# Kernel tuning notes

Measured on AMD Instinct MI355X. Metric: run time of the kernel, lower is better.

The kernel has to match this reference:

```python
import jax, jax.numpy as jnp
import numpy as np

BATCH, LENGTH, IN, STATE, OUT = 8, 4096, 512, 256, 512


def setup_inputs() -> dict:
    key = jax.random.key(0)
    k1, k2, k3, k4, k5 = jax.random.split(key, 5)
    u = jax.random.normal(k1, (BATCH, LENGTH, IN), dtype=jnp.float32)
    x0 = jax.random.normal(k2, (BATCH, STATE), dtype=jnp.float32)
    A = 0.9999 * (2.0 * jax.random.uniform(k3, (STATE,), dtype=jnp.float32) - 1.0)
    B = jax.random.normal(k4, (IN, STATE), dtype=jnp.float32) / (STATE + IN) ** 0.5
    C = jax.random.normal(k5, (STATE, OUT), dtype=jnp.float32) / STATE ** 0.5
    return {"u": u, "x0": x0, "A": A, "B": B, "C": C}


def reference(u, x0, A, B, C):
    L = u.shape[1]
    # A_powers[t, n] = A[n] ** t, shape [L, state]
    A_powers = jnp.power(A[None, :], jnp.arange(L, dtype=u.dtype)[:, None])
    uB = u @ B  # [batch, L, state]
    # FFT convolution; inputs are real so rfft/irfft gives same result as
    # real(ifft(fft*fft)) in the original.
    T = 2 ** int(np.ceil(np.log2(2 * L - 1)))
    Af = jnp.fft.rfft(A_powers, n=T, axis=0)  # [T/2+1, state]
    Uf = jnp.fft.rfft(uB, n=T, axis=1)        # [batch, T/2+1, state]
    x = jnp.fft.irfft(Af[None, :, :] * Uf, n=T, axis=1)[:, :L]  # [batch, L, state]
    # initial-state contribution: A * A_powers * x0
    x = x + A[None, None, :] * A_powers[None, :, :] * x0[:, None, :]
    y = x @ C  # [batch, L, out]
    return (y, x[:, -1])
```

## Files before the change

kernel.cpp:

```cpp
#include <hip/hip_runtime.h>

#define BATCH   8
#define LENGTH  4096
#define IN_DIM  512
#define STATE   256
#define OUT_DIM 512
#define NC      64
#define LC      64

typedef __attribute__((ext_vector_type(8))) short bf16x8;
typedef __attribute__((ext_vector_type(4))) float f32x4;

union FragU { bf16x8 v; unsigned u[4]; };

__device__ __forceinline__ unsigned short bf16_rne(float v) {
    unsigned u = __builtin_bit_cast(unsigned, v);
    unsigned r = (u + 0x7FFFu + ((u >> 16) & 1u)) >> 16;
    return (unsigned short)r;
}
__device__ __forceinline__ float bf16_f(unsigned short h) {
    unsigned u = ((unsigned)h) << 16;
    return __builtin_bit_cast(float, u);
}

__global__ __launch_bounds__(256) void split_T_kernel(
    const float* __restrict__ in, unsigned short* __restrict__ hi,
    unsigned short* __restrict__ lo, int kbits, int Nsrc)
{
    int id = blockIdx.x * 256 + threadIdx.x;
    int k = id & ((1 << kbits) - 1);
    int n = id >> kbits;
    float v = in[(size_t)k * Nsrc + n];
    unsigned short h = bf16_rne(v);
    hi[id] = h;
    lo[id] = bf16_rne(v - bf16_f(h));
}

__global__ __launch_bounds__(512, 4) void gemm_dbuf(
    const float* __restrict__ Af, const unsigned short* __restrict__ Bthi,
    const unsigned short* __restrict__ Btlo, float* __restrict__ Cc,
    int N_, int K)
{
    __shared__ unsigned short lds[2 * 16384];

    const int tid  = threadIdx.x;
    const int wave = tid >> 6;
    const int lane = tid & 63;
    const int n0 = blockIdx.x * 128;
    const int m0 = blockIdx.y * 128;

    const char* gp[4];
    int ldsoff[4], gstep[4];
    #pragma unroll
    for (int t = 0; t < 4; ++t) {
        int gi = wave * 4 + t;
        if (gi < 16) {
            int p = gi * 64 + lane;
            int row = p >> 3, s = p & 7;
            int l = s ^ (row & 7);
            gp[t] = (const char*)(Af + (size_t)(m0 + row) * K + l * 4);
            gstep[t] = 32 * 4;
            ldsoff[t] = gi * 512;
        } else {
            int q2 = (gi - 16) >> 3;
            int pi = gi & 7;
            int p = pi * 64 + lane;
            int row = p >> 2, s = p & 3;
            int l = s ^ ((row >> 1) & 3);
            const unsigned short* base = q2 ? Btlo : Bthi;
            gp[t] = (const char*)(base + (size_t)(n0 + row) * K + l * 8);
            gstep[t] = 32 * 2;
            ldsoff[t] = 8192 + q2 * 4096 + pi * 512;
        }
    }

    const int r = lane & 15, q = lane >> 4;
    const int wm = (wave >> 2) * 64, wn = (wave & 3) * 32;

    int aoff[4][2], boff[2];
    #pragma unroll
    for (int i = 0; i < 4; ++i) {
        int row = wm + i * 16 + r;
        #pragma unroll
        for (int h = 0; h < 2; ++h)
            aoff[i][h] = row * 64 + ((2 * q + h) ^ (row & 7)) * 8;
    }
    #pragma unroll
    for (int j = 0; j < 2; ++j) {
        int row = wn + j * 16 + r;
        boff[j] = row * 32 + (q ^ ((row >> 1) & 3)) * 8;
    }

    f32x4 acc[4][2];
    #pragma unroll
    for (int i = 0; i < 4; ++i)
        #pragma unroll
        for (int j = 0; j < 2; ++j)
            acc[i][j] = (f32x4){0.f, 0.f, 0.f, 0.f};

    #pragma unroll
    for (int t = 0; t < 4; ++t) {
        __builtin_amdgcn_global_load_lds(
            (const __attribute__((address_space(1))) unsigned*)(gp[t]),
            (__attribute__((address_space(3))) unsigned*)(&lds[ldsoff[t]]),
            16, 0, 0);
        gp[t] += gstep[t];
    }

    const int nit = K >> 5;
    for (int it = 0; it < nit; ++it) {
        asm volatile("" ::: "memory");
        __builtin_amdgcn_s_barrier();
        asm volatile("" ::: "memory");
        if (it + 1 < nit) {
            const int bb = ((it + 1) & 1) * 16384;
            #pragma unroll
            for (int t = 0; t < 4; ++t) {
                __builtin_amdgcn_global_load_lds(
                    (const __attribute__((address_space(1))) unsigned*)(gp[t]),
                    (__attribute__((address_space(3))) unsigned*)(&lds[bb + ldsoff[t]]),
                    16, 0, 0);
                gp[t] += gstep[t];
            }
            __builtin_amdgcn_s_waitcnt(0x0F74);
        } else {
            __builtin_amdgcn_s_waitcnt(0x0F70);
        }
        asm volatile("" ::: "memory");
        __builtin_amdgcn_s_barrier();
        asm volatile("" ::: "memory");

        const unsigned short* buf = &lds[(it & 1) * 16384];

        FragU ahi[4], alo[4];
        #pragma unroll
        for (int i = 0; i < 4; ++i) {
            #pragma unroll
            for (int h = 0; h < 2; ++h) {
                float4 f = *(const float4*)(buf + aoff[i][h]);
                unsigned bx = __builtin_bit_cast(unsigned, f.x);
                unsigned by = __builtin_bit_cast(unsigned, f.y);
                unsigned bz = __builtin_bit_cast(unsigned, f.z);
                unsigned bw = __builtin_bit_cast(unsigned, f.w);
                ahi[i].u[h * 2]     = __builtin_amdgcn_perm(by, bx, 0x07060302);
                ahi[i].u[h * 2 + 1] = __builtin_amdgcn_perm(bw, bz, 0x07060302);
                float lx = f.x - __builtin_bit_cast(float, bx & 0xFFFF0000u);
                float ly = f.y - __builtin_bit_cast(float, by & 0xFFFF0000u);
                float lz = f.z - __builtin_bit_cast(float, bz & 0xFFFF0000u);
                float lw = f.w - __builtin_bit_cast(float, bw & 0xFFFF0000u);
                alo[i].u[h * 2]     = __builtin_amdgcn_perm(
                    __builtin_bit_cast(unsigned, ly), __builtin_bit_cast(unsigned, lx), 0x07060302);
                alo[i].u[h * 2 + 1] = __builtin_amdgcn_perm(
                    __builtin_bit_cast(unsigned, lw), __builtin_bit_cast(unsigned, lz), 0x07060302);
            }
        }
        FragU bhi[2], blo[2];
        #pragma unroll
        for (int j = 0; j < 2; ++j) {
            bhi[j].v = *(const bf16x8*)(buf +  8192 + boff[j]);
            blo[j].v = *(const bf16x8*)(buf + 12288 + boff[j]);
        }
        #pragma unroll
        for (int i = 0; i < 4; ++i)
            #pragma unroll
            for (int j = 0; j < 2; ++j) {
                acc[i][j] = __builtin_amdgcn_mfma_f32_16x16x32_bf16(ahi[i].v, bhi[j].v, acc[i][j], 0, 0, 0);
                acc[i][j] = __builtin_amdgcn_mfma_f32_16x16x32_bf16(alo[i].v, bhi[j].v, acc[i][j], 0, 0, 0);
                acc[i][j] = __builtin_amdgcn_mfma_f32_16x16x32_bf16(ahi[i].v, blo[j].v, acc[i][j], 0, 0, 0);
            }
    }

    #pragma unroll
    for (int i = 0; i < 4; ++i) {
        #pragma unroll
        for (int reg = 0; reg < 4; ++reg) {
            int mg = m0 + wm + i * 16 + q * 4 + reg;
            float* dst = Cc + (size_t)mg * N_ + n0 + wn + r;
            dst[0]  = acc[i][0][reg];
            dst[16] = acc[i][1][reg];
        }
    }
}

__global__ __launch_bounds__(256) void scan_carry(
    const float* __restrict__ uB, const float* __restrict__ A,
    float* __restrict__ carry)
{
    const int b = blockIdx.x;
    const int c = blockIdx.y;
    const int n = threadIdx.x;
    const float a = A[n];
    const float* p = uB + ((size_t)b * LENGTH + (size_t)c * LC) * STATE + n;
    float s = 0.f;
    #pragma unroll 8
    for (int j = 0; j < LC; ++j) s = a * s + p[(size_t)j * STATE];
    carry[((size_t)b * NC + c) * STATE + n] = s;
}

__global__ __launch_bounds__(256) void scan_apply(
    const float* __restrict__ uB, const float* __restrict__ A,
    const float* __restrict__ carry, const float* __restrict__ x0,
    float* __restrict__ x, float* __restrict__ x_last)
{
    const int b = blockIdx.x;
    const int c = blockIdx.y;
    const int n = threadIdx.x;
    const float a = A[n];
    float a2 = a * a, a4 = a2 * a2, a8 = a4 * a4, a16 = a8 * a8, a32 = a16 * a16;
    const float aLC = a32 * a32;

    float s = x0[(size_t)b * STATE + n];
    for (int d = 0; d < c; ++d)
        s = aLC * s + carry[((size_t)b * NC + d) * STATE + n];

    const size_t base = ((size_t)b * LENGTH + (size_t)c * LC) * STATE + n;
    const float* p = uB + base;
    float* qx = x + base;
    #pragma unroll 8
    for (int j = 0; j < LC; ++j) {
        s = a * s + p[(size_t)j * STATE];
        qx[(size_t)j * STATE] = s;
    }
    if (c == NC - 1) x_last[(size_t)b * STATE + n] = s;
}

extern "C" void kernel_launch(void* const* d_in, const int* in_sizes, int n_in,
                              void* d_out, int out_size, void* d_ws, size_t ws_size,
                              hipStream_t stream)
{
    const float* u  = (const float*)d_in[0];
    const float* x0 = (const float*)d_in[1];
    const float* A  = (const float*)d_in[2];
    const float* B  = (const float*)d_in[3];
    const float* C  = (const float*)d_in[4];

    const size_t MB = 1024 * 1024;
    char* ws = (char*)d_ws;

    float* x     = (float*)(ws);
    float* carry = (float*)(ws + 32 * MB);
    unsigned short* Bt_hi = (unsigned short*)(ws + 33 * MB);
    unsigned short* Bt_lo = (unsigned short*)(ws + 33 * MB + 256 * 1024);
    unsigned short* Ct_hi = (unsigned short*)(ws + 33 * MB + 512 * 1024);
    unsigned short* Ct_lo = (unsigned short*)(ws + 33 * MB + 768 * 1024);

    float* y      = (float*)d_out;
    float* x_last = y + (size_t)BATCH * LENGTH * OUT_DIM;
    float* uB     = (float*)((char*)d_out + 32 * MB);

    const int M = BATCH * LENGTH;

    split_T_kernel<<<dim3((IN_DIM * STATE) / 256), dim3(256), 0, stream>>>(B, Bt_hi, Bt_lo, 9, STATE);
    split_T_kernel<<<dim3((STATE * OUT_DIM) / 256), dim3(256), 0, stream>>>(C, Ct_hi, Ct_lo, 8, OUT_DIM);

    gemm_dbuf<<<dim3(STATE / 128, M / 128), dim3(512), 0, stream>>>(
        u, Bt_hi, Bt_lo, uB, STATE, IN_DIM);

    scan_carry<<<dim3(BATCH, NC), dim3(256), 0, stream>>>(uB, A, carry);
    scan_apply<<<dim3(BATCH, NC), dim3(256), 0, stream>>>(uB, A, carry, x0, x, x_last);

    gemm_dbuf<<<dim3(OUT_DIM / 128, M / 128), dim3(512), 0, stream>>>(
        x, Ct_hi, Ct_lo, y, OUT_DIM, STATE);
}
```

Measured before the change: 209.2 us.

## Switch GEMM to 32x32x16 MFMA with 4 waves per block

The GEMM block drops from 8 waves to 4. Each wave now computes a 64x64 tile with 32x32x16 bf16 MFMAs instead of 16x16x32 ones, and each thread issues 8 global-to-LDS loads per stage instead of 4. Larger MFMA tiles mean fewer LDS fragment reads per flop and fewer instructions. The cost is more accumulator registers, fewer waves to hide latency, and a strided epilogue store pattern.

```diff
diff --git a/kernel.cpp b/kernel.cpp
--- a/kernel.cpp
+++ b/kernel.cpp
@@ -8,8 +8,8 @@
 #define NC      64
 #define LC      64
 
-typedef __attribute__((ext_vector_type(8))) short bf16x8;
-typedef __attribute__((ext_vector_type(4))) float f32x4;
+typedef __attribute__((ext_vector_type(8)))  short bf16x8;
+typedef __attribute__((ext_vector_type(16))) float f32x16;
 
 union FragU { bf16x8 v; unsigned u[4]; };
 
@@ -36,7 +36,7 @@
     lo[id] = bf16_rne(v - bf16_f(h));
 }
 
-__global__ __launch_bounds__(512, 4) void gemm_dbuf(
+__global__ __launch_bounds__(256, 2) void gemm_dbuf(
     const float* __restrict__ Af, const unsigned short* __restrict__ Bthi,
     const unsigned short* __restrict__ Btlo, float* __restrict__ Cc,
     int N_, int K)
@@ -49,11 +49,11 @@
     const int n0 = blockIdx.x * 128;
     const int m0 = blockIdx.y * 128;
 
-    const char* gp[4];
-    int ldsoff[4], gstep[4];
-    #pragma unroll
-    for (int t = 0; t < 4; ++t) {
-        int gi = wave * 4 + t;
+    const char* gp[8];
+    int ldsoff[8], gstep[8];
+    #pragma unroll
+    for (int t = 0; t < 8; ++t) {
+        int gi = wave * 8 + t;
         if (gi < 16) {
             int p = gi * 64 + lane;
             int row = p >> 3, s = p & 7;
@@ -63,7 +63,7 @@
             ldsoff[t] = gi * 512;
         } else {
             int q2 = (gi - 16) >> 3;
-            int pi = gi & 7;
+            int pi = (gi - 16) & 7;
             int p = pi * 64 + lane;
             int row = p >> 2, s = p & 3;
             int l = s ^ ((row >> 1) & 3);
@@ -74,32 +74,38 @@
         }
     }
 
-    const int r = lane & 15, q = lane >> 4;
-    const int wm = (wave >> 2) * 64, wn = (wave & 3) * 32;
-
-    int aoff[4][2], boff[2];
-    #pragma unroll
-    for (int i = 0; i < 4; ++i) {
-        int row = wm + i * 16 + r;
-        #pragma unroll
-        for (int h = 0; h < 2; ++h)
-            aoff[i][h] = row * 64 + ((2 * q + h) ^ (row & 7)) * 8;
-    }
-    #pragma unroll
-    for (int j = 0; j < 2; ++j) {
-        int row = wn + j * 16 + r;
-        boff[j] = row * 32 + (q ^ ((row >> 1) & 3)) * 8;
-    }
-
-    f32x4 acc[4][2];
-    #pragma unroll
-    for (int i = 0; i < 4; ++i)
-        #pragma unroll
-        for (int j = 0; j < 2; ++j)
-            acc[i][j] = (f32x4){0.f, 0.f, 0.f, 0.f};
-
-    #pragma unroll
-    for (int t = 0; t < 4; ++t) {
+    const int l31 = lane & 31, q2 = lane >> 5;
+    const int wm = (wave >> 1) * 64, wn = (wave & 1) * 64;
+
+    int aoff[2][2][2];
+    #pragma unroll
+    for (int mi = 0; mi < 2; ++mi) {
+        int row = wm + mi * 32 + l31;
+        #pragma unroll
+        for (int ks = 0; ks < 2; ++ks)
+            #pragma unroll
+            for (int h = 0; h < 2; ++h)
+                aoff[mi][ks][h] = row * 64 + ((ks * 4 + q2 * 2 + h) ^ (row & 7)) * 8;
+    }
+    int boff[2][2];
+    #pragma unroll
+    for (int nj = 0; nj < 2; ++nj) {
+        int row = wn + nj * 32 + l31;
+        #pragma unroll
+        for (int ks = 0; ks < 2; ++ks)
+            boff[nj][ks] = row * 32 + (((ks * 2 + q2) ^ ((row >> 1) & 3))) * 8;
+    }
+
+    f32x16 acc[2][2];
+    #pragma unroll
+    for (int mi = 0; mi < 2; ++mi)
+        #pragma unroll
+        for (int nj = 0; nj < 2; ++nj)
+            #pragma unroll
+            for (int r = 0; r < 16; ++r) acc[mi][nj][r] = 0.f;
+
+    #pragma unroll
+    for (int t = 0; t < 8; ++t) {
         __builtin_amdgcn_global_load_lds(
             (const __attribute__((address_space(1))) unsigned*)(gp[t]),
             (__attribute__((address_space(3))) unsigned*)(&lds[ldsoff[t]]),
@@ -115,14 +121,14 @@
         if (it + 1 < nit) {
             const int bb = ((it + 1) & 1) * 16384;
             #pragma unroll
-            for (int t = 0; t < 4; ++t) {
+            for (int t = 0; t < 8; ++t) {
                 __builtin_amdgcn_global_load_lds(
                     (const __attribute__((address_space(1))) unsigned*)(gp[t]),
                     (__attribute__((address_space(3))) unsigned*)(&lds[bb + ldsoff[t]]),
                     16, 0, 0);
                 gp[t] += gstep[t];
             }
-            __builtin_amdgcn_s_waitcnt(0x0F74);
+            __builtin_amdgcn_s_waitcnt(0x0F78);
         } else {
             __builtin_amdgcn_s_waitcnt(0x0F70);
         }
@@ -132,54 +138,73 @@
 
         const unsigned short* buf = &lds[(it & 1) * 16384];
 
-        FragU ahi[4], alo[4];
-        #pragma unroll
-        for (int i = 0; i < 4; ++i) {
-            #pragma unroll
-            for (int h = 0; h < 2; ++h) {
-                float4 f = *(const float4*)(buf + aoff[i][h]);
-                unsigned bx = __builtin_bit_cast(unsigned, f.x);
-                unsigned by = __builtin_bit_cast(unsigned, f.y);
-                unsigned bz = __builtin_bit_cast(unsigned, f.z);
-                unsigned bw = __builtin_bit_cast(unsigned, f.w);
-                ahi[i].u[h * 2]     = __builtin_amdgcn_perm(by, bx, 0x07060302);
-                ahi[i].u[h * 2 + 1] = __builtin_amdgcn_perm(bw, bz, 0x07060302);
-                float lx = f.x - __builtin_bit_cast(float, bx & 0xFFFF0000u);
-                float ly = f.y - __builtin_bit_cast(float, by & 0xFFFF0000u);
-                float lz = f.z - __builtin_bit_cast(float, bz & 0xFFFF0000u);
-                float lw = f.w - __builtin_bit_cast(float, bw & 0xFFFF0000u);
-                alo[i].u[h * 2]     = __builtin_amdgcn_perm(
-                    __builtin_bit_cast(unsigned, ly), __builtin_bit_cast(unsigned, lx), 0x07060302);
-                alo[i].u[h * 2 + 1] = __builtin_amdgcn_perm(
-                    __builtin_bit_cast(unsigned, lw), __builtin_bit_cast(unsigned, lz), 0x07060302);
-            }
-        }
-        FragU bhi[2], blo[2];
-        #pragma unroll
-        for (int j = 0; j < 2; ++j) {
-            bhi[j].v = *(const bf16x8*)(buf +  8192 + boff[j]);
-            blo[j].v = *(const bf16x8*)(buf + 12288 + boff[j]);
-        }
-        #pragma unroll
-        for (int i = 0; i < 4; ++i)
-            #pragma unroll
-            for (int j = 0; j < 2; ++j) {
-                acc[i][j] = __builtin_amdgcn_mfma_f32_16x16x32_bf16(ahi[i].v, bhi[j].v, acc[i][j], 0, 0, 0);
-                acc[i][j] = __builtin_amdgcn_mfma_f32_16x16x32_bf16(alo[i].v, bhi[j].v, acc[i][j], 0, 0, 0);
-                acc[i][j] = __builtin_amdgcn_mfma_f32_16x16x32_bf16(ahi[i].v, blo[j].v, acc[i][j], 0, 0, 0);
-            }
-    }
-
-    #pragma unroll
-    for (int i = 0; i < 4; ++i) {
-        #pragma unroll
-        for (int reg = 0; reg < 4; ++reg) {
-            int mg = m0 + wm + i * 16 + q * 4 + reg;
-            float* dst = Cc + (size_t)mg * N_ + n0 + wn + r;
-            dst[0]  = acc[i][0][reg];
-            dst[16] = acc[i][1][reg];
-        }
-    }
+        #pragma unroll
+        for (int ks = 0; ks < 2; ++ks) {
+            FragU ahi[2], alo[2];
+            #pragma unroll
+            for (int mi = 0; mi < 2; ++mi) {
+                float4 f0 = *(const float4*)(buf + aoff[mi][ks][0]);
+                float4 f1 = *(const float4*)(buf + aoff[mi][ks][1]);
+                unsigned b0 = __builtin_bit_cast(unsigned, f0.x);
+                unsigned b1 = __builtin_bit_cast(unsigned, f0.y);
+                unsigned b2 = __builtin_bit_cast(unsigned, f0.z);
+                unsigned b3 = __builtin_bit_cast(unsigned, f0.w);
+                unsigned b4 = __builtin_bit_cast(unsigned, f1.x);
+                unsigned b5 = __builtin_bit_cast(unsigned, f1.y);
+                unsigned b6 = __builtin_bit_cast(unsigned, f1.z);
+                unsigned b7 = __builtin_bit_cast(unsigned, f1.w);
+                ahi[mi].u[0] = __builtin_amdgcn_perm(b1, b0, 0x07060302);
+                ahi[mi].u[1] = __builtin_amdgcn_perm(b3, b2, 0x07060302);
+                ahi[mi].u[2] = __builtin_amdgcn_perm(b5, b4, 0x07060302);
+                ahi[mi].u[3] = __builtin_amdgcn_perm(b7, b6, 0x07060302);
+                float l0 = f0.x - __builtin_bit_cast(float, b0 & 0xFFFF0000u);
+                float l1 = f0.y - __builtin_bit_cast(float, b1 & 0xFFFF0000u);
+                float l2 = f0.z - __builtin_bit_cast(float, b2 & 0xFFFF0000u);
+                float l3 = f0.w - __builtin_bit_cast(float, b3 & 0xFFFF0000u);
+                float l4 = f1.x - __builtin_bit_cast(float, b4 & 0xFFFF0000u);
+                float l5 = f1.y - __builtin_bit_cast(float, b5 & 0xFFFF0000u);
+                float l6 = f1.z - __builtin_bit_cast(float, b6 & 0xFFFF0000u);
+                float l7 = f1.w - __builtin_bit_cast(float, b7 & 0xFFFF0000u);
+                alo[mi].u[0] = __builtin_amdgcn_perm(
+                    __builtin_bit_cast(unsigned, l1), __builtin_bit_cast(unsigned, l0), 0x07060302);
+                alo[mi].u[1] = __builtin_amdgcn_perm(
+                    __builtin_bit_cast(unsigned, l3), __builtin_bit_cast(unsigned, l2), 0x07060302);
+                alo[mi].u[2] = __builtin_amdgcn_perm(
+                    __builtin_bit_cast(unsigned, l5), __builtin_bit_cast(unsigned, l4), 0x07060302);
+                alo[mi].u[3] = __builtin_amdgcn_perm(
+                    __builtin_bit_cast(unsigned, l7), __builtin_bit_cast(unsigned, l6), 0x07060302);
+            }
+            FragU bhi[2], blo[2];
+            #pragma unroll
+            for (int nj = 0; nj < 2; ++nj) {
+                bhi[nj].v = *(const bf16x8*)(buf +  8192 + boff[nj][ks]);
+                blo[nj].v = *(const bf16x8*)(buf + 12288 + boff[nj][ks]);
+            }
+            #pragma unroll
+            for (int mi = 0; mi < 2; ++mi)
+                #pragma unroll
+                for (int nj = 0; nj < 2; ++nj) {
+                    acc[mi][nj] = __builtin_amdgcn_mfma_f32_32x32x16_bf16(
+                        ahi[mi].v, bhi[nj].v, acc[mi][nj], 0, 0, 0);
+                    acc[mi][nj] = __builtin_amdgcn_mfma_f32_32x32x16_bf16(
+                        alo[mi].v, bhi[nj].v, acc[mi][nj], 0, 0, 0);
+                    acc[mi][nj] = __builtin_amdgcn_mfma_f32_32x32x16_bf16(
+                        ahi[mi].v, blo[nj].v, acc[mi][nj], 0, 0, 0);
+                }
+        }
+    }
+
+    #pragma unroll
+    for (int mi = 0; mi < 2; ++mi)
+        #pragma unroll
+        for (int nj = 0; nj < 2; ++nj) {
+            #pragma unroll
+            for (int r = 0; r < 16; ++r) {
+                int row_g = m0 + wm + mi * 32 + 4 * q2 + (r & 3) + 8 * (r >> 2);
+                int col_g = n0 + wn + nj * 32 + l31;
+                Cc[(size_t)row_g * N_ + col_g] = acc[mi][nj][r];
+            }
+        }
 }
 
 __global__ __launch_bounds__(256) void scan_carry(
@@ -253,12 +278,12 @@
     split_T_kernel<<<dim3((IN_DIM * STATE) / 256), dim3(256), 0, stream>>>(B, Bt_hi, Bt_lo, 9, STATE);
     split_T_kernel<<<dim3((STATE * OUT_DIM) / 256), dim3(256), 0, stream>>>(C, Ct_hi, Ct_lo, 8, OUT_DIM);
 
-    gemm_dbuf<<<dim3(STATE / 128, M / 128), dim3(512), 0, stream>>>(
+    gemm_dbuf<<<dim3(STATE / 128, M / 128), dim3(256), 0, stream>>>(
         u, Bt_hi, Bt_lo, uB, STATE, IN_DIM);
 
     scan_carry<<<dim3(BATCH, NC), dim3(256), 0, stream>>>(uB, A, carry);
     scan_apply<<<dim3(BATCH, NC), dim3(256), 0, stream>>>(uB, A, carry, x0, x, x_last);
 
-    gemm_dbuf<<<dim3(OUT_DIM / 128, M / 128), dim3(512), 0, stream>>>(
+    gemm_dbuf<<<dim3(OUT_DIM / 128, M / 128), dim3(256), 0, stream>>>(
         x, Ct_hi, Ct_lo, y, OUT_DIM, STATE);
 }
```

Result: slower. 217.0 us (+3.7%).
